# Kernel tuning notes

Hardware: AMD Instinct MI355X
Metric: run time of the kernel (lower is better)

The kernel has to match this reference:

```python
import jax, jax.numpy as jnp
import numpy as np

# BERT-base geometry
B, N, H, DH = 4, 512, 12, 64
HID = H * DH            # 768
E = 65536               # total edges (~avg degree 32)
NREL = 64               # relation vocabulary


def setup_inputs() -> dict:
    key = jax.random.key(0)
    ks = jax.random.split(key, 12)
    node_states = jax.random.normal(ks[0], (B, N, HID), jnp.float32)
    b = jax.random.randint(ks[1], (E,), 0, B)
    hn = jax.random.randint(ks[2], (E,), 0, N)
    tn = jax.random.randint(ks[3], (E,), 0, N)
    r = jax.random.randint(ks[4], (E,), 0, NREL)
    edge_indices = jnp.stack([b, hn, tn, r]).astype(jnp.int32)  # (4, E)
    node_type_ids = jnp.zeros((B, N), jnp.int32)  # unused by this subclass
    sc = 0.02
    Wq = jax.random.normal(ks[5], (HID, HID), jnp.float32) * sc
    bq = jnp.zeros((HID,), jnp.float32)
    Wk = jax.random.normal(ks[6], (HID, HID), jnp.float32) * sc
    bk = jnp.zeros((HID,), jnp.float32)
    Wv = jax.random.normal(ks[7], (HID, HID), jnp.float32) * sc
    bv = jnp.zeros((HID,), jnp.float32)
    # relation matrix embeddings: one (DH, DH) matrix per relation id
    rel_emb = jnp.eye(DH, dtype=jnp.float32)[None] + jax.random.normal(ks[8], (NREL, DH, DH), jnp.float32) * sc
    return {"node_states": node_states, "edge_indices": edge_indices,
            "node_type_ids": node_type_ids, "Wq": Wq, "bq": bq,
            "Wk": Wk, "bk": bk, "Wv": Wv, "bv": bv, "rel_emb": rel_emb}


def reference(node_states, edge_indices, node_type_ids, Wq, bq, Wk, bk, Wv, bv, rel_emb):
    Bq, Nn, hid = node_states.shape
    # dense QKV projections (torch Linear: y = x @ W^T + b)
    Q = node_states @ Wq.T + bq
    K = node_states @ Wk.T + bk
    V = (node_states @ Wv.T + bv).reshape(Bq, Nn, H, DH)  # (B,N,H,D)
    be, he, te, re = edge_indices  # each (E,)
    # per-edge gathers
    Qe = Q[be, he].reshape(-1, H, DH)   # (E,H,D)
    Ke = K[be, te].reshape(-1, H, DH)   # (E,H,D)
    Re = rel_emb[re]                     # (E,D,D) relation matrix per edge
    # Q projected through relation matrix, then inner product with K per head
    Qp = jnp.einsum('ehd,edk->ehk', Qe, Re)
    logits = jnp.einsum('ehd,ehd->eh', Qp, Ke) / jnp.sqrt(jnp.float32(DH))  # (E,H)
    # sparse softmax over tail nodes: segment = (batch, head_node)
    seg = be * Nn + he
    nseg = Bq * Nn
    m = jax.ops.segment_max(logits, seg, num_segments=nseg)      # (BN,H)
    ex = jnp.exp(logits - m[seg])
    denom = jax.ops.segment_sum(ex, seg, num_segments=nseg)      # (BN,H)
    p = ex / denom[seg]                                          # (E,H)
    # dropout prob = 0.0 (deterministic reference)
    # aggregate: out[b,i,h,:] = sum_edges p_e * V[b, tail_e, h, :]
    contrib = p[:, :, None] * V[be, te]                          # (E,H,D)
    out = jax.ops.segment_sum(contrib, seg, num_segments=nseg)   # (BN,H,D)
    return out.reshape(Bq, Nn, H * DH)
```

## Files before the change

### kernel.cpp

```cpp
#include <hip/hip_runtime.h>
#include <hip/hip_bf16.h>

#define NB   4
#define NN   512
#define NH   12
#define DHD  64
#define HID  768
#define NE   65536
#define NSEG 2048
#define NREL 64
#define LGS  16
#define SCAP 128
#define NSUB2 8
#define RSUB (NREL * NSUB2)
#define RCAP 256
#define RLY2 12
#define POISON 0xAAAAAAAAu

typedef short bf16x8 __attribute__((ext_vector_type(8)));
typedef float f32x4  __attribute__((ext_vector_type(4)));
typedef unsigned short u16x8 __attribute__((ext_vector_type(8)));

__device__ __forceinline__ unsigned short f2bf(float f) {
    __hip_bfloat16 h = __float2bfloat16(f);
    return *reinterpret_cast<unsigned short*>(&h);
}
__device__ __forceinline__ float bf2f(unsigned short s) {
    return __int_as_float(((int)s) << 16);
}
__device__ __forceinline__ int unpz(int v) {
    return (int)((unsigned)v - POISON);
}
__device__ __forceinline__ void load_lds16(const void* g, void* l) {
    __builtin_amdgcn_global_load_lds(
        (const __attribute__((address_space(1))) unsigned int*)g,
        (__attribute__((address_space(3))) unsigned int*)l, 16, 0, 0);
}

#define NX4 ((2048 * 768) / 4)
#define NW4 ((768 * 768) / 4)
#define NCAST ((NX4 + 3 * NW4) / 256)
__global__ __launch_bounds__(256) void cast_scatter_kernel(
    const float* __restrict__ X, const float* __restrict__ Wq,
    const float* __restrict__ Wk, const float* __restrict__ Wv,
    unsigned short* __restrict__ Xh, unsigned short* __restrict__ Wh,
    const int* __restrict__ ei,
    int* __restrict__ cursor, int* __restrict__ rcursor,
    int* __restrict__ s_te, int* __restrict__ s_pkr)
{
    if (blockIdx.x >= NCAST) {
        const int e = (blockIdx.x - NCAST) * 256 + threadIdx.x;
        const int b  = ei[e];
        const int hn = ei[NE + e];
        const int tn = ei[2 * NE + e];
        const int rr = ei[3 * NE + e];
        const int seg = b * NN + hn;
        const int slot = unpz(atomicAdd(&cursor[seg], 1)) & (SCAP - 1);
        const int pos  = seg * SCAP + slot;
        s_te[pos] = tn;
        const int rsub = rr * NSUB2 + ((e >> 8) & (NSUB2 - 1));
        const int rj = unpz(atomicAdd(&rcursor[rsub], 1)) & (RCAP - 1);
        int2 pv2; pv2.x = (seg << 9) | tn; pv2.y = pos;
        ((int2*)s_pkr)[rsub * RCAP + rj] = pv2;
        return;
    }
    const int i = blockIdx.x * 256 + threadIdx.x;
    float4 v;
    ushort4* dst;
    if (i < NX4) {
        v = ((const float4*)X)[i];
        dst = &((ushort4*)Xh)[i];
    } else {
        const int j = i - NX4;
        const float* W = (j < NW4) ? Wq : ((j < 2 * NW4) ? Wk : Wv);
        const int jj = (j < NW4) ? j : ((j < 2 * NW4) ? j - NW4 : j - 2 * NW4);
        v = ((const float4*)W)[jj];
        dst = &((ushort4*)Wh)[j];
    }
    ushort4 r;
    r.x = f2bf(v.x); r.y = f2bf(v.y); r.z = f2bf(v.z); r.w = f2bf(v.w);
    *dst = r;
}

#define NQKV 576
__global__ __launch_bounds__(256) void qkv_kernel(
    const unsigned short* __restrict__ Xh, const unsigned short* __restrict__ Wh,
    const float* __restrict__ bq, const float* __restrict__ bk,
    const float* __restrict__ bv,
    unsigned short* __restrict__ Qh, unsigned short* __restrict__ Kh,
    unsigned short* __restrict__ Vh)
{
    __shared__ __align__(16) char smem[64 * 132 * 4];
    const int tid = threadIdx.x;

    const int gb  = blockIdx.x;
    const int bid = (gb & 7) * 72 + (gb >> 3);
    const int z   = bid / 192;
    const int rem = bid - z * 192;
    const int by  = rem / 6;
    const int bx  = rem - by * 6;
    const unsigned short* W = Wh + (size_t)z * (768 * 768);
    const float* bias = (z == 0) ? bq : ((z == 1) ? bk : bv);

    const int n0 = bx * 128;
    const int m0 = by * 64;
    const int lane = tid & 63;
    const int wave = tid >> 6;
    const int wm = wave >> 1, wn = wave & 1;

    unsigned short* As = (unsigned short*)smem;
    unsigned short* Bs = (unsigned short*)(smem + 8192);
    float* Cs = (float*)smem;

    f32x4 acc[2][4];
    #pragma unroll
    for (int a = 0; a < 2; ++a)
        #pragma unroll
        for (int b2 = 0; b2 < 4; ++b2) acc[a][b2] = (f32x4){0.f, 0.f, 0.f, 0.f};

    const int ml = lane & 15;
    const int q4 = lane >> 4;

    for (int k0 = 0; k0 < HID; k0 += 64) {
        __syncthreads();
        #pragma unroll
        for (int i = 0; i < 2; ++i) {
            const int slotb = i * 256 + wave * 64;
            const int idx = slotb + lane;
            const int row = idx >> 3;
            const int kq  = (idx & 7) ^ (row & 7);
            load_lds16(Xh + (size_t)(m0 + row) * HID + k0 + kq * 8,
                       As + slotb * 8);
        }
        #pragma unroll
        for (int i = 0; i < 4; ++i) {
            const int slotb = i * 256 + wave * 64;
            const int idx = slotb + lane;
            const int row = idx >> 3;
            const int kq  = (idx & 7) ^ (row & 7);
            load_lds16(W + (size_t)(n0 + row) * HID + k0 + kq * 8,
                       Bs + slotb * 8);
        }
        __syncthreads();

        #pragma unroll
        for (int ks = 0; ks < 2; ++ks) {
            bf16x8 af[2], bfr[4];
            #pragma unroll
            for (int t = 0; t < 2; ++t) {
                const int ar = wm * 32 + t * 16 + ml;
                const int ac = (ks * 4 + q4) ^ (ar & 7);
                af[t] = *(const bf16x8*)(As + ar * 64 + ac * 8);
            }
            #pragma unroll
            for (int t = 0; t < 4; ++t) {
                const int br = wn * 64 + t * 16 + ml;
                const int bc = (ks * 4 + q4) ^ (br & 7);
                bfr[t] = *(const bf16x8*)(Bs + br * 64 + bc * 8);
            }
            #pragma unroll
            for (int mt = 0; mt < 2; ++mt)
                #pragma unroll
                for (int nt = 0; nt < 4; ++nt)
                    acc[mt][nt] = __builtin_amdgcn_mfma_f32_16x16x32_bf16(
                        af[mt], bfr[nt], acc[mt][nt], 0, 0, 0);
        }
    }

    __syncthreads();
    #pragma unroll
    for (int mt = 0; mt < 2; ++mt)
        #pragma unroll
        for (int nt = 0; nt < 4; ++nt)
            #pragma unroll
            for (int rg = 0; rg < 4; ++rg)
                Cs[(wm * 32 + mt * 16 + q4 * 4 + rg) * 132 +
                   wn * 64 + nt * 16 + ml] = acc[mt][nt][rg];
    __syncthreads();

    unsigned short* Y = (z == 0) ? Qh : ((z == 1) ? Kh : Vh);
    #pragma unroll
    for (int it = 0; it < 4; ++it) {
        const int id  = tid + it * 256;
        const int row = id >> 4;
        const int cg  = id & 15;
        const float* cp = Cs + row * 132 + cg * 8;
        const float4 cA = *(const float4*)cp;
        const float4 cB = *(const float4*)(cp + 4);
        const float* bp = bias + n0 + cg * 8;
        const float4 bA = *(const float4*)bp;
        const float4 bB = *(const float4*)(bp + 4);
        const size_t o = (size_t)(m0 + row) * HID + n0 + cg * 8;
        u16x8 r;
        r[0] = f2bf(cA.x + bA.x); r[1] = f2bf(cA.y + bA.y);
        r[2] = f2bf(cA.z + bA.z); r[3] = f2bf(cA.w + bA.w);
        r[4] = f2bf(cB.x + bB.x); r[5] = f2bf(cB.y + bB.y);
        r[6] = f2bf(cB.z + bB.z); r[7] = f2bf(cB.w + bB.w);
        *(u16x8*)&Y[o] = r;
    }
}

__global__ __launch_bounds__(256) void rel_logits(
    const unsigned short* __restrict__ Qh, const unsigned short* __restrict__ Kh,
    const float* __restrict__ rel,
    const int* __restrict__ rcursor, const int* __restrict__ s_pkr,
    float* __restrict__ Lg)
{
    const int rs = blockIdx.x;
    int cnt = unpz(rcursor[rs]);
    cnt = (cnt < 0) ? 0 : ((cnt > RCAP) ? RCAP : cnt);
    const int rows = cnt * NH;
    if ((int)blockIdx.y * 256 >= rows) return;
    const int r = rs >> 3;
    const int tid = threadIdx.x;
    const int lane = tid & 63;
    const int wave = tid >> 6;

    __shared__ int qb[256], kb[256], oi[256];
    __shared__ float QpS[4][16][68];
    __shared__ __align__(16) unsigned short frS[4096];

    {
        const float* Rg = rel + (size_t)r * 4096;
        #pragma unroll
        for (int it = 0; it < 4; ++it) {
            const int i4 = it * 256 + tid;
            const float4 v4 = ((const float4*)Rg)[i4];
            const int d  = i4 >> 4;
            const int c0 = (i4 & 15) * 4;
            const int ks = d >> 5, q4 = (d >> 3) & 3, j = d & 7;
            const float vv[4] = {v4.x, v4.y, v4.z, v4.w};
            #pragma unroll
            for (int e = 0; e < 4; ++e) {
                const int c = c0 + e, nt = c >> 4, n = c & 15;
                frS[((ks * 4 + nt) * 64 + q4 * 16 + n) * 8 + j] = f2bf(vv[e]);
            }
        }
    }
    __syncthreads();
    bf16x8 bfrag[2][4];
    #pragma unroll
    for (int ks = 0; ks < 2; ++ks)
        #pragma unroll
        for (int nt = 0; nt < 4; ++nt)
            bfrag[ks][nt] = *(const bf16x8*)(frS + ((ks * 4 + nt) * 64 + lane) * 8);

    for (int t0 = blockIdx.y * 256; t0 < rows; t0 += RLY2 * 256) {
        __syncthreads();
        {
            const int rowid = t0 + tid;
            if (rowid < rows) {
                const int el = rowid / 12;
                const int h  = rowid - el * 12;
                const int2 v = ((const int2*)s_pkr)[rs * RCAP + el];
                const int pos = v.y & (NSEG * SCAP - 1);
                const int sg  = (v.x >> 9) & (NSEG - 1);
                const int te  = v.x & (NN - 1);
                qb[tid] = sg * HID + h * 64;
                kb[tid] = ((sg & ~(NN - 1)) + te) * HID + h * 64;
                oi[tid] = pos * LGS + h;
            } else { qb[tid] = 0; kb[tid] = 0; oi[tid] = -1; }
        }
        __syncthreads();

        const int rw = lane >> 2, ch = (lane & 3) * 16;
        bf16x8 kv0[4], kv1[4];
        #pragma unroll
        for (int gi = 0; gi < 4; ++gi) {
            const int kbase = kb[(wave + gi * 4) * 16 + rw];
            kv0[gi] = *(const bf16x8*)(Kh + kbase + ch);
            kv1[gi] = *(const bf16x8*)(Kh + kbase + ch + 8);
        }

        #pragma unroll
        for (int gi = 0; gi < 4; ++gi) {
            const int g = wave + gi * 4;
            const int m = lane & 15, q4 = lane >> 4;
            const int qbase = qb[g * 16 + m];
            f32x4 cfr[4] = {{0,0,0,0},{0,0,0,0},{0,0,0,0},{0,0,0,0}};
            #pragma unroll
            for (int ks = 0; ks < 2; ++ks) {
                const bf16x8 afr = *(const bf16x8*)(Qh + qbase + ks * 32 + q4 * 8);
                #pragma unroll
                for (int nt = 0; nt < 4; ++nt)
                    cfr[nt] = __builtin_amdgcn_mfma_f32_16x16x32_bf16(
                        afr, bfrag[ks][nt], cfr[nt], 0, 0, 0);
            }
            #pragma unroll
            for (int nt = 0; nt < 4; ++nt)
                #pragma unroll
                for (int rg = 0; rg < 4; ++rg)
                    QpS[wave][q4 * 4 + rg][nt * 16 + m] = cfr[nt][rg];

            const int rowid2 = g * 16 + rw;
            float s = 0.f;
            #pragma unroll
            for (int i = 0; i < 8; ++i) {
                s = fmaf(QpS[wave][rw][ch + i],     bf2f((unsigned short)kv0[gi][i]), s);
                s = fmaf(QpS[wave][rw][ch + 8 + i], bf2f((unsigned short)kv1[gi][i]), s);
            }
            s += __shfl_xor(s, 1, 64);
            s += __shfl_xor(s, 2, 64);
            if ((lane & 3) == 0) {
                const int o = oi[rowid2];
                if (o >= 0) Lg[o] = __expf(s * 0.125f);
            }
        }
    }
}

__global__ __launch_bounds__(256) void seg_softmax_agg(
    const unsigned short* __restrict__ Vh, const float* __restrict__ Lg,
    const int* __restrict__ s_te,
    float* __restrict__ out,
    int* __restrict__ cursor, int* __restrict__ rcursor)
{
    const int seg  = blockIdx.x;
    const int tid  = threadIdx.x;
    int cnt = unpz(cursor[seg]);
    __syncthreads();
    if (tid == 0) {
        cursor[seg] = (int)POISON;
        if (seg < RSUB) rcursor[seg] = (int)POISON;
    }
    cnt = (cnt < 0) ? 0 : ((cnt > SCAP) ? SCAP : cnt);
    const int base = seg * SCAP;
    const int lane = tid & 63;
    const int w    = tid >> 6;
    const int browbase = seg & ~(NN - 1);

    __shared__ int   te_s[64];
    __shared__ float pv[4][3][64];

    float l0 = 0.f, l1 = 0.f, l2 = 0.f;
    float acc0 = 0.f, acc1 = 0.f, acc2 = 0.f;

    for (int c0 = 0; c0 < cnt; c0 += 64) {
        const int cc = min(64, cnt - c0);
        __syncthreads();
        if (tid < 64)
            te_s[tid] = (tid < cc) ? (s_te[base + c0 + tid] & (NN - 1)) : 0;
        __syncthreads();

        float p0 = 0.f, p1 = 0.f, p2 = 0.f;
        if (lane < cc) {
            const float* Lp = Lg + (size_t)(base + c0 + lane) * LGS;
            p0 = Lp[w]; p1 = Lp[4 + w]; p2 = Lp[8 + w];
        }
        float s0 = p0, s1 = p1, s2 = p2;
        #pragma unroll
        for (int o = 1; o < 64; o <<= 1) {
            s0 += __shfl_xor(s0, o, 64);
            s1 += __shfl_xor(s1, o, 64);
            s2 += __shfl_xor(s2, o, 64);
        }
        l0 += s0; l1 += s1; l2 += s2;
        pv[w][0][lane] = p0; pv[w][1][lane] = p1; pv[w][2][lane] = p2;

        for (int j0 = 0; j0 < cc; j0 += 4) {
            float vb0[4], vb1[4], vb2[4];
            #pragma unroll
            for (int u = 0; u < 4; ++u) {
                const unsigned short* __restrict__ Vr =
                    Vh + (size_t)(browbase + te_s[(j0 + u) & 63]) * HID + lane;
                vb0[u] = bf2f(Vr[w * 64]);
                vb1[u] = bf2f(Vr[(4 + w) * 64]);
                vb2[u] = bf2f(Vr[(8 + w) * 64]);
            }
            #pragma unroll
            for (int u = 0; u < 4; ++u) {
                const int j = j0 + u;
                acc0 = fmaf(pv[w][0][j & 63], vb0[u], acc0);
                acc1 = fmaf(pv[w][1][j & 63], vb1[u], acc1);
                acc2 = fmaf(pv[w][2][j & 63], vb2[u], acc2);
            }
        }
    }

    float* Yo = out + (size_t)seg * HID;
    Yo[tid]       = (l0 > 0.f) ? acc0 / l0 : 0.f;
    Yo[tid + 256] = (l1 > 0.f) ? acc1 / l1 : 0.f;
    Yo[tid + 512] = (l2 > 0.f) ? acc2 / l2 : 0.f;
}

extern "C" void kernel_launch(void* const* d_in, const int* in_sizes, int n_in,
                              void* d_out, int out_size, void* d_ws, size_t ws_size,
                              hipStream_t stream)
{
    const float* X   = (const float*)d_in[0];
    const int*   EI  = (const int*)d_in[1];
    const float* Wq  = (const float*)d_in[3];
    const float* bq  = (const float*)d_in[4];
    const float* Wk  = (const float*)d_in[5];
    const float* bk  = (const float*)d_in[6];
    const float* Wv  = (const float*)d_in[7];
    const float* bv  = (const float*)d_in[8];
    const float* rel = (const float*)d_in[9];
    float* out = (float*)d_out;

    char* p = (char*)d_ws;
    unsigned short* Qh = (unsigned short*)p;  p += (size_t)NSEG * HID * 2;
    unsigned short* Kh = (unsigned short*)p;  p += (size_t)NSEG * HID * 2;
    unsigned short* Vh = (unsigned short*)p;  p += (size_t)NSEG * HID * 2;
    float* Lg = (float*)p;                    p += (size_t)NSEG * SCAP * LGS * 4;
    unsigned short* Xh = (unsigned short*)p;  p += (size_t)NB * NN * HID * 2;
    unsigned short* Wh = (unsigned short*)p;  p += (size_t)3 * 768 * 768 * 2;
    int* cursor   = (int*)p;                  p += NSEG * 4;
    int* rcursor  = (int*)p;                  p += RSUB * 4;
    int* s_te     = (int*)p;                  p += (size_t)NSEG * SCAP * 4;
    int* s_pkr    = (int*)p;                  p += (size_t)RSUB * RCAP * 8;

    cast_scatter_kernel<<<NCAST + 256, 256, 0, stream>>>(
        X, Wq, Wk, Wv, Xh, Wh, EI, cursor, rcursor, s_te, s_pkr);
    qkv_kernel<<<NQKV, 256, 0, stream>>>(
        Xh, Wh, bq, bk, bv, Qh, Kh, Vh);
    rel_logits<<<dim3(RSUB, RLY2), 256, 0, stream>>>(
        Qh, Kh, rel, rcursor, s_pkr, Lg);
    seg_softmax_agg<<<NSEG, 256, 0, stream>>>(
        Vh, Lg, s_te, out, cursor, rcursor);
}
```

Measured before the change: 171.6 us.

## Map one wave per segment in softmax-aggregate and shrink rel_logits grid

The softmax-aggregation kernel now gives each of the four waves in a block its own segment, so the grid is a quarter the size. Each lane loads four bf16 V values at once and accumulates float4s, and the per-chunk block barriers are gone because LDS staging is now private to each wave. Softmax denominators for all 12 heads are kept per lane and reduced with one butterfly at the end. The y-dimension of the rel_logits grid also drops from 12 to 2, which only stays correct if that kernel strides its work by gridDim.y; it trades parallelism for less per-block overhead.

New measurement: 166.5 us. 1.03x faster.

```diff
diff --git a/kernel.cpp b/kernel.cpp
--- a/kernel.cpp
+++ b/kernel.cpp
@@ -14,7 +14,7 @@
 #define NSUB2 8
 #define RSUB (NREL * NSUB2)
 #define RCAP 256
-#define RLY2 12
+#define RLY2 2
 #define POISON 0xAAAAAAAAu
 
 typedef short bf16x8 __attribute__((ext_vector_type(8)));
@@ -315,72 +315,92 @@
     float* __restrict__ out,
     int* __restrict__ cursor, int* __restrict__ rcursor)
 {
-    const int seg  = blockIdx.x;
     const int tid  = threadIdx.x;
+    const int lane = tid & 63;
+    const int w    = tid >> 6;
+    const int seg  = blockIdx.x * 4 + w;
+
     int cnt = unpz(cursor[seg]);
     __syncthreads();
-    if (tid == 0) {
-        cursor[seg] = (int)POISON;
-        if (seg < RSUB) rcursor[seg] = (int)POISON;
-    }
+    if (tid < 4) cursor[blockIdx.x * 4 + tid] = (int)POISON;
+    if (blockIdx.x < RSUB / 4 && tid < 4)
+        rcursor[blockIdx.x * 4 + tid] = (int)POISON;
     cnt = (cnt < 0) ? 0 : ((cnt > SCAP) ? SCAP : cnt);
+
     const int base = seg * SCAP;
-    const int lane = tid & 63;
-    const int w    = tid >> 6;
     const int browbase = seg & ~(NN - 1);
-
-    __shared__ int   te_s[64];
-    __shared__ float pv[4][3][64];
-
-    float l0 = 0.f, l1 = 0.f, l2 = 0.f;
-    float acc0 = 0.f, acc1 = 0.f, acc2 = 0.f;
+    const int h0 = lane >> 4;
+
+    __shared__ float pjS[4][12][68];
+    __shared__ int   teS[4][64];
+
+    float4 acc[3] = {{0,0,0,0},{0,0,0,0},{0,0,0,0}};
+    float dl[12];
+    #pragma unroll
+    for (int h = 0; h < 12; ++h) dl[h] = 0.f;
 
     for (int c0 = 0; c0 < cnt; c0 += 64) {
         const int cc = min(64, cnt - c0);
-        __syncthreads();
-        if (tid < 64)
-            te_s[tid] = (tid < cc) ? (s_te[base + c0 + tid] & (NN - 1)) : 0;
-        __syncthreads();
-
-        float p0 = 0.f, p1 = 0.f, p2 = 0.f;
+        float4 pA = {0,0,0,0}, pB = {0,0,0,0}, pC = {0,0,0,0};
+        int te = 0;
         if (lane < cc) {
             const float* Lp = Lg + (size_t)(base + c0 + lane) * LGS;
-            p0 = Lp[w]; p1 = Lp[4 + w]; p2 = Lp[8 + w];
-        }
-        float s0 = p0, s1 = p1, s2 = p2;
-        #pragma unroll
-        for (int o = 1; o < 64; o <<= 1) {
-            s0 += __shfl_xor(s0, o, 64);
-            s1 += __shfl_xor(s1, o, 64);
-            s2 += __shfl_xor(s2, o, 64);
-        }
-        l0 += s0; l1 += s1; l2 += s2;
-        pv[w][0][lane] = p0; pv[w][1][lane] = p1; pv[w][2][lane] = p2;
-
-        for (int j0 = 0; j0 < cc; j0 += 4) {
-            float vb0[4], vb1[4], vb2[4];
-            #pragma unroll
-            for (int u = 0; u < 4; ++u) {
-                const unsigned short* __restrict__ Vr =
-                    Vh + (size_t)(browbase + te_s[(j0 + u) & 63]) * HID + lane;
-                vb0[u] = bf2f(Vr[w * 64]);
-                vb1[u] = bf2f(Vr[(4 + w) * 64]);
-                vb2[u] = bf2f(Vr[(8 + w) * 64]);
-            }
-            #pragma unroll
-            for (int u = 0; u < 4; ++u) {
-                const int j = j0 + u;
-                acc0 = fmaf(pv[w][0][j & 63], vb0[u], acc0);
-                acc1 = fmaf(pv[w][1][j & 63], vb1[u], acc1);
-                acc2 = fmaf(pv[w][2][j & 63], vb2[u], acc2);
-            }
-        }
-    }
-
-    float* Yo = out + (size_t)seg * HID;
-    Yo[tid]       = (l0 > 0.f) ? acc0 / l0 : 0.f;
-    Yo[tid + 256] = (l1 > 0.f) ? acc1 / l1 : 0.f;
-    Yo[tid + 512] = (l2 > 0.f) ? acc2 / l2 : 0.f;
+            pA = *(const float4*)(Lp);
+            pB = *(const float4*)(Lp + 4);
+            pC = *(const float4*)(Lp + 8);
+            te = s_te[base + c0 + lane] & (NN - 1);
+        }
+        teS[w][lane] = te;
+        pjS[w][0][lane]  = pA.x; pjS[w][1][lane]  = pA.y;
+        pjS[w][2][lane]  = pA.z; pjS[w][3][lane]  = pA.w;
+        pjS[w][4][lane]  = pB.x; pjS[w][5][lane]  = pB.y;
+        pjS[w][6][lane]  = pB.z; pjS[w][7][lane]  = pB.w;
+        pjS[w][8][lane]  = pC.x; pjS[w][9][lane]  = pC.y;
+        pjS[w][10][lane] = pC.z; pjS[w][11][lane] = pC.w;
+        dl[0] += pA.x; dl[1] += pA.y; dl[2]  += pA.z; dl[3]  += pA.w;
+        dl[4] += pB.x; dl[5] += pB.y; dl[6]  += pB.z; dl[7]  += pB.w;
+        dl[8] += pC.x; dl[9] += pC.y; dl[10] += pC.z; dl[11] += pC.w;
+
+        for (int j = 0; j < cc; ++j) {
+            const int row = browbase + teS[w][j];
+            const unsigned short* Vr = Vh + (size_t)row * HID + (lane << 2);
+            const ushort4 v0 = *(const ushort4*)(Vr);
+            const ushort4 v1 = *(const ushort4*)(Vr + 256);
+            const ushort4 v2 = *(const ushort4*)(Vr + 512);
+            const float p0 = pjS[w][h0][j];
+            const float p1 = pjS[w][4 + h0][j];
+            const float p2 = pjS[w][8 + h0][j];
+            acc[0].x = fmaf(p0, bf2f(v0.x), acc[0].x);
+            acc[0].y = fmaf(p0, bf2f(v0.y), acc[0].y);
+            acc[0].z = fmaf(p0, bf2f(v0.z), acc[0].z);
+            acc[0].w = fmaf(p0, bf2f(v0.w), acc[0].w);
+            acc[1].x = fmaf(p1, bf2f(v1.x), acc[1].x);
+            acc[1].y = fmaf(p1, bf2f(v1.y), acc[1].y);
+            acc[1].z = fmaf(p1, bf2f(v1.z), acc[1].z);
+            acc[1].w = fmaf(p1, bf2f(v1.w), acc[1].w);
+            acc[2].x = fmaf(p2, bf2f(v2.x), acc[2].x);
+            acc[2].y = fmaf(p2, bf2f(v2.y), acc[2].y);
+            acc[2].z = fmaf(p2, bf2f(v2.z), acc[2].z);
+            acc[2].w = fmaf(p2, bf2f(v2.w), acc[2].w);
+        }
+    }
+
+    #pragma unroll
+    for (int o = 1; o < 64; o <<= 1) {
+        #pragma unroll
+        for (int h = 0; h < 12; ++h) dl[h] += __shfl_xor(dl[h], o, 64);
+    }
+    float* Yo = out + (size_t)seg * HID + (lane << 2);
+    #pragma unroll
+    for (int k = 0; k < 3; ++k) {
+        const float d = dl[k * 4 + h0];
+        float4 r;
+        r.x = (d > 0.f) ? acc[k].x / d : 0.f;
+        r.y = (d > 0.f) ? acc[k].y / d : 0.f;
+        r.z = (d > 0.f) ? acc[k].z / d : 0.f;
+        r.w = (d > 0.f) ? acc[k].w / d : 0.f;
+        *(float4*)(Yo + k * 256) = r;
+    }
 }
 
 extern "C" void kernel_launch(void* const* d_in, const int* in_sizes, int n_in,
@@ -416,6 +436,6 @@
         Xh, Wh, bq, bk, bv, Qh, Kh, Vh);
     rel_logits<<<dim3(RSUB, RLY2), 256, 0, stream>>>(
         Qh, Kh, rel, rcursor, s_pkr, Lg);
-    seg_softmax_agg<<<NSEG, 256, 0, stream>>>(
+    seg_softmax_agg<<<NSEG / 4, 256, 0, stream>>>(
         Vh, Lg, s_te, out, cursor, rcursor);
 }
```
